# Kernel tuning notes

Measured on AMD Instinct MI355X. Metric: run time of the kernel, lower is better.

The kernel has to match this reference:

```python
import jax, jax.numpy as jnp
import numpy as np

EPS = 1e-5


def setup_inputs() -> dict:
    key = jax.random.key(0)
    k_u, k_v, k_w, k_g, k_b, k_m, k_var = jax.random.split(key, 7)
    B, S, C1, C2, H, W = 4, 8, 64, 64, 128, 128
    CC = C1 + C2  # concat channels = out channels = 128
    u = jax.random.normal(k_u, (B, 1, C1, H, W), dtype=jnp.float32)
    v = jax.random.normal(k_v, (B, S, C2, H, W), dtype=jnp.float32)
    conv_w = jax.random.normal(k_w, (CC, CC, 3, 3), dtype=jnp.float32) * 0.05  # OIHW
    bn_gamma = jnp.ones((CC,), jnp.float32) + 0.1 * jax.random.normal(k_g, (CC,), dtype=jnp.float32)
    bn_beta = 0.1 * jax.random.normal(k_b, (CC,), dtype=jnp.float32)
    bn_mean = 0.1 * jax.random.normal(k_m, (CC,), dtype=jnp.float32)
    bn_var = jnp.abs(jax.random.normal(k_var, (CC,), dtype=jnp.float32)) + 0.5
    return {"u": u, "v": v, "conv_w": conv_w, "bn_gamma": bn_gamma,
            "bn_beta": bn_beta, "bn_mean": bn_mean, "bn_var": bn_var}


def _cross_conv(u, v, conv_w, bn_gamma, bn_beta, bn_mean, bn_var):
    B, _, C1, H, W = u.shape
    _, S, C2, _, _ = v.shape
    # broadcast u over the s axis, concat channels -> (b*s, c1+c2, h, w)
    us = jnp.broadcast_to(u[:, 0, None], (B, S, C1, H, W))
    xy = jnp.concatenate([us, v], axis=2).reshape(B * S, C1 + C2, H, W)
    # 3x3 conv, stride 1, SAME padding, no bias (BN follows)
    y = jax.lax.conv_general_dilated(
        xy, conv_w, window_strides=(1, 1), padding=((1, 1), (1, 1)),
        dimension_numbers=("NCHW", "OIHW", "NCHW"))
    # BatchNorm (inference: running stats)
    scale = (bn_gamma * jax.lax.rsqrt(bn_var + EPS))[None, :, None, None]
    shift = (bn_beta - bn_mean * bn_gamma * jax.lax.rsqrt(bn_var + EPS))[None, :, None, None]
    y = y * scale + shift
    # skip = Identity (concat_channels == out_channels, stride 1), then ReLU
    out = jax.nn.relu(y + xy)
    return out.reshape(B, 1, S, C1 + C2, H, W)


def reference(u, v, conv_w, bn_gamma, bn_beta, bn_mean, bn_var):
    return _cross_conv(u, v, conv_w, bn_gamma, bn_beta, bn_mean, bn_var)
```

## Files before the change

### kernel.cpp

```cpp
#include <hip/hip_runtime.h>
#include <hip/hip_bf16.h>


#define EPS 1e-5f

typedef __attribute__((ext_vector_type(8))) short short8;
typedef __attribute__((ext_vector_type(4))) float f32x4;
typedef __attribute__((ext_vector_type(2))) float f32x2;

constexpr int C1 = 64, CC = 128, Hd = 128, Wd = 128;
constexpr int HW = Hd * Wd;
constexpr int TW = 16, TH = 8;
constexpr int SPW = 18, SPH = 10;
constexpr int ROW = 40;
constexpr int WFRAGS = 9 * 4 * 8;
constexpr int NTHR = 256;
constexpr int UNITS = 16 * SPH * 10;
constexpr int NU = (UNITS + NTHR - 1) / NTHR;

__global__ void prep_weights(const float* __restrict__ wgt, ushort* __restrict__ wf) {
    int idx = blockIdx.x * 256 + threadIdx.x;
    if (idx >= WFRAGS * 64) return;
    int l  = idx & 63;
    int f  = idx >> 6;
    int cf = f & 7;
    int c  = (f >> 3) & 3;
    int t  = f >> 5;
    int kh = t / 3, kw = t % 3;
    int co  = cf * 16 + (l & 15);
    int cib = c * 32 + (l >> 4) * 8;
    ushort* dst = wf + (size_t)idx * 8;
#pragma unroll
    for (int j = 0; j < 8; ++j) {
        float x = wgt[(((size_t)co * CC + cib + j) * 3 + kh) * 3 + kw];
        __hip_bfloat16 bb = __float2bfloat16(x);
        dst[j] = *(ushort*)&bb;
    }
}

__global__ __launch_bounds__(NTHR, 3)
void crossconv_mfma(const float* __restrict__ u,
                    const float* __restrict__ v,
                    const ushort* __restrict__ wf,
                    const float* __restrict__ gamma,
                    const float* __restrict__ beta,
                    const float* __restrict__ mean,
                    const float* __restrict__ var,
                    float* __restrict__ out) {
    __shared__ alignas(16) ushort in_s[2][SPH * SPW * ROW];
    __shared__ float s_sc[CC], s_sh[CC];

    const int tid = threadIdx.x;
    const int w0 = blockIdx.x * TW;
    const int h0 = blockIdx.y * TH;
    const int n  = blockIdx.z;
    const int b  = n >> 3;
    const float* __restrict__ ubase = u + (size_t)b * C1 * HW;
    const float* __restrict__ vbase = v + (size_t)n * C1 * HW;

    if (tid < CC) {
        float sc = gamma[tid] * rsqrtf(var[tid] + EPS);
        s_sc[tid] = sc;
        s_sh[tid] = beta[tid] - mean[tid] * sc;
    }
    {
        uint4 z{0u, 0u, 0u, 0u};
        uint4* p = (uint4*)&in_s[0][0];
        for (int i = tid; i < 2 * SPH * SPW * ROW * 2 / 16; i += NTHR) p[i] = z;
    }

    const int l = tid & 63, wid = tid >> 6;
    const int n16 = l & 15, kgrp = l >> 4;

    int  goff[NU];
    int  sidx[NU];
    uint lm = 0, m0 = 0, m1 = 0;
#pragma unroll
    for (int i = 0; i < NU; ++i) {
        goff[i] = 0; sidx[i] = ROW;
        int e = tid + i * NTHR;
        if (e < UNITS) {
            int cp  = e / 100;
            int r   = e - cp * 100;
            int sph = r / 10;
            int j   = r - sph * 10;
            int gh  = h0 + sph - 1;
            int gw  = w0 + 2 * j - 2;
            sidx[i] = (sph * SPW + 2 * j) * ROW + 2 * cp;
            if ((unsigned)gh < (unsigned)Hd && (unsigned)gw < (unsigned)(Wd - 1)) {
                goff[i] = 2 * cp * HW + gh * Wd + gw;
                lm |= 1u << i;
                if (j >= 1) m0 |= 1u << i;
                if (j <= 8) m1 |= 1u << i;
            }
        }
    }

    f32x4 acc[2][8];
#pragma unroll
    for (int cfl = 0; cfl < 2; ++cfl)
#pragma unroll
        for (int pf = 0; pf < 8; ++pf) acc[cfl][pf] = (f32x4)0.f;

    f32x2 sa[NU], sb[NU];

    auto chunk_src = [&](int c) -> const float* {
        return (c < 2) ? ubase + (size_t)c * 32 * HW
                       : vbase + (size_t)(c - 2) * 32 * HW;
    };
    auto stage_load = [&](const float* __restrict__ src) {
#pragma unroll
        for (int i = 0; i < NU; ++i) {
            sa[i] = f32x2{0.f, 0.f}; sb[i] = f32x2{0.f, 0.f};
            if (lm & (1u << i)) {
                const float* p = src + goff[i];
                sa[i] = *(const f32x2*)p;
                sb[i] = *(const f32x2*)(p + HW);
            }
        }
    };
    auto stage_write = [&](int buf) {
        ushort* __restrict__ d = in_s[buf];
#pragma unroll
        for (int i = 0; i < NU; ++i) {
            __hip_bfloat16 ax = __float2bfloat16(sa[i].x);
            __hip_bfloat16 bx = __float2bfloat16(sb[i].x);
            __hip_bfloat16 ay = __float2bfloat16(sa[i].y);
            __hip_bfloat16 by = __float2bfloat16(sb[i].y);
            uint v0 = (uint)*(ushort*)&ax | ((uint)*(ushort*)&bx << 16);
            uint v1 = (uint)*(ushort*)&ay | ((uint)*(ushort*)&by << 16);
            if (m0 & (1u << i)) *(uint*)&d[sidx[i] - ROW] = v0;
            if (m1 & (1u << i)) *(uint*)&d[sidx[i]]       = v1;
        }
    };
    auto compute = [&](int buf, int c) {
        const ushort* __restrict__ bs = in_s[buf];
#pragma unroll
        for (int t = 0; t < 9; ++t) {
            const int kh = t / 3, kw = t % 3;
            const int spw = n16 + kw;
            const short8* __restrict__ wp =
                (const short8*)wf + ((size_t)((t * 4 + c) * 8 + wid * 2)) * 64 + l;
            short8 wf0 = wp[0];
            short8 wf1 = wp[64];
#pragma unroll
            for (int pf = 0; pf < 8; ++pf) {
                short8 p = *(const short8*)&bs[((pf + kh) * SPW + spw) * ROW + kgrp * 8];
                acc[0][pf] = __builtin_amdgcn_mfma_f32_16x16x32_bf16(p, wf0, acc[0][pf], 0, 0, 0);
                acc[1][pf] = __builtin_amdgcn_mfma_f32_16x16x32_bf16(p, wf1, acc[1][pf], 0, 0, 0);
            }
        }
    };

    stage_load(chunk_src(0));
    __syncthreads();
    stage_write(0);
    __syncthreads();

#pragma unroll
    for (int c = 0; c < 4; ++c) {
        if (c < 3) stage_load(chunk_src(c + 1));
        compute(c & 1, c);
        if (c < 3) stage_write((c & 1) ^ 1);
        __syncthreads();
    }

#pragma unroll
    for (int cfl = 0; cfl < 2; ++cfl) {
        const int co = (wid * 2 + cfl) * 16 + n16;
        const float sc = s_sc[co], sh = s_sh[co];
        const float* __restrict__ xb = (co < C1) ? (ubase + (size_t)co * HW)
                                                 : (vbase + (size_t)(co - C1) * HW);
        float* __restrict__ ob = out + ((size_t)n * CC + co) * HW;
#pragma unroll
        for (int pf = 0; pf < 8; ++pf) {
            const int off = (h0 + pf) * Wd + w0 + kgrp * 4;
            f32x4 x = *(const f32x4*)(xb + off);
            f32x4 a = acc[cfl][pf];
            f32x4 y;
#pragma unroll
            for (int r = 0; r < 4; ++r)
                y[r] = fmaxf(fmaf(a[r], sc, sh) + x[r], 0.f);
            *(f32x4*)(ob + off) = y;
        }
    }
}

extern "C" void kernel_launch(void* const* d_in, const int* in_sizes, int n_in,
                              void* d_out, int out_size, void* d_ws, size_t ws_size,
                              hipStream_t stream) {
    const float* u     = (const float*)d_in[0];
    const float* v     = (const float*)d_in[1];
    const float* wgt   = (const float*)d_in[2];
    const float* gamma = (const float*)d_in[3];
    const float* beta  = (const float*)d_in[4];
    const float* mean  = (const float*)d_in[5];
    const float* var   = (const float*)d_in[6];
    float* out = (float*)d_out;
    ushort* wf = (ushort*)d_ws;

    prep_weights<<<dim3((WFRAGS * 64 + 255) / 256), dim3(256), 0, stream>>>(wgt, wf);
    crossconv_mfma<<<dim3(Wd / TW, Hd / TH, 32), dim3(NTHR), 0, stream>>>(
        u, v, wf, gamma, beta, mean, var, out);
}
```

Measured before the change: 929.7 us.

## Pack staging offsets into one register, swizzle block order, stop unrolling chunk loop

Merges the per-unit global offset and shared-memory index into a single packed 32-bit register, and derives the load mask from the existing write masks, to cut register pressure. Removes full unrolling of the four-chunk main loop, likely to shrink code and registers. Also remaps the linear block index so consecutive workgroups land on different samples/tiles, which changes L2 locality and the spread of work across XCDs. The packing relies on the global offset fitting in 19 bits. The rolled loop adds dynamic indexing of the shared buffer and source pointer.

New measurement: 908.6 us. 1.02x faster.

```diff
diff --git a/kernel.cpp b/kernel.cpp
--- a/kernel.cpp
+++ b/kernel.cpp
@@ -51,9 +51,11 @@
     __shared__ float s_sc[CC], s_sh[CC];
 
     const int tid = threadIdx.x;
-    const int w0 = blockIdx.x * TW;
-    const int h0 = blockIdx.y * TH;
-    const int n  = blockIdx.z;
+    const int lin  = blockIdx.x + 8 * blockIdx.y + 128 * blockIdx.z;
+    const int orig = (lin & 7) * 512 + (lin >> 3);
+    const int w0 = (orig & 7) * TW;
+    const int h0 = ((orig >> 3) & 15) * TH;
+    const int n  = orig >> 7;
     const int b  = n >> 3;
     const float* __restrict__ ubase = u + (size_t)b * C1 * HW;
     const float* __restrict__ vbase = v + (size_t)n * C1 * HW;
@@ -72,12 +74,11 @@
     const int l = tid & 63, wid = tid >> 6;
     const int n16 = l & 15, kgrp = l >> 4;
 
-    int  goff[NU];
-    int  sidx[NU];
-    uint lm = 0, m0 = 0, m1 = 0;
+    uint pk[NU];
+    uint m0 = 0, m1 = 0;
 #pragma unroll
     for (int i = 0; i < NU; ++i) {
-        goff[i] = 0; sidx[i] = ROW;
+        pk[i] = ROW;
         int e = tid + i * NTHR;
         if (e < UNITS) {
             int cp  = e / 100;
@@ -86,12 +87,13 @@
             int j   = r - sph * 10;
             int gh  = h0 + sph - 1;
             int gw  = w0 + 2 * j - 2;
-            sidx[i] = (sph * SPW + 2 * j) * ROW + 2 * cp;
+            uint sidx = (sph * SPW + 2 * j) * ROW + 2 * cp;
             if ((unsigned)gh < (unsigned)Hd && (unsigned)gw < (unsigned)(Wd - 1)) {
-                goff[i] = 2 * cp * HW + gh * Wd + gw;
-                lm |= 1u << i;
+                pk[i] = ((uint)(2 * cp * HW + gh * Wd + gw) << 13) | sidx;
                 if (j >= 1) m0 |= 1u << i;
                 if (j <= 8) m1 |= 1u << i;
+            } else {
+                pk[i] = sidx;
             }
         }
     }
@@ -109,11 +111,12 @@
                        : vbase + (size_t)(c - 2) * 32 * HW;
     };
     auto stage_load = [&](const float* __restrict__ src) {
+        const uint lm = m0 | m1;
 #pragma unroll
         for (int i = 0; i < NU; ++i) {
             sa[i] = f32x2{0.f, 0.f}; sb[i] = f32x2{0.f, 0.f};
             if (lm & (1u << i)) {
-                const float* p = src + goff[i];
+                const float* p = src + (pk[i] >> 13);
                 sa[i] = *(const f32x2*)p;
                 sb[i] = *(const f32x2*)(p + HW);
             }
@@ -129,8 +132,9 @@
             __hip_bfloat16 by = __float2bfloat16(sb[i].y);
             uint v0 = (uint)*(ushort*)&ax | ((uint)*(ushort*)&bx << 16);
             uint v1 = (uint)*(ushort*)&ay | ((uint)*(ushort*)&by << 16);
-            if (m0 & (1u << i)) *(uint*)&d[sidx[i] - ROW] = v0;
-            if (m1 & (1u << i)) *(uint*)&d[sidx[i]]       = v1;
+            int si = (int)(pk[i] & 8191u);
+            if (m0 & (1u << i)) *(uint*)&d[si - ROW] = v0;
+            if (m1 & (1u << i)) *(uint*)&d[si]       = v1;
         }
     };
     auto compute = [&](int buf, int c) {
@@ -157,7 +161,6 @@
     stage_write(0);
     __syncthreads();
 
-#pragma unroll
     for (int c = 0; c < 4; ++c) {
         if (c < 3) stage_load(chunk_src(c + 1));
         compute(c & 1, c);
```
